# Optimization experiments

Measured on AMD Instinct MI355X. Metric: run time of the kernel, lower is better.

The kernel has to match this reference:

```python
import jax, jax.numpy as jnp
import numpy as np

N_NODES = 100000
N_EDGES = 3200000
ALPHA_KCL = 1.0
ALPHA_KVL = 1.0
EPS = 1e-6


def setup_inputs() -> dict:
    key = jax.random.key(0)
    k1, k2, k3, k4 = jax.random.split(key, 4)
    node_features = jax.random.normal(k1, (N_NODES, 4), dtype=jnp.float32)
    edge_index = jax.random.randint(k2, (2, N_EDGES), 0, N_NODES, dtype=jnp.int64)
    edge_logits = jax.random.normal(k3, (N_EDGES,), dtype=jnp.float32)
    edge_params = jax.random.uniform(k4, (N_EDGES, 2), dtype=jnp.float32)
    return {
        "node_features": node_features,
        "edge_index": edge_index,
        "edge_logits": edge_logits,
        "edge_params": edge_params,
    }


def reference(node_features, edge_index, edge_logits, edge_params):
    n_nodes = node_features.shape[0]
    edge_probs = jax.nn.sigmoid(edge_logits)  # [E]
    src = edge_index[0]  # [E]
    dst = edge_index[1]  # [E]
    v = node_features[:, 0]  # [N] voltage column
    # per-edge current: |v_src - v_dst| / (R + X + eps) * prob
    v_diff = jnp.abs(v[src] - v[dst])
    impedance = edge_params[:, 0] + edge_params[:, 1]
    current = v_diff / (impedance + EPS) * edge_probs  # [E]
    # KCL: each edge subtracts its current at src, adds at dst
    node_sum = (
        jax.ops.segment_sum(current, dst, num_segments=n_nodes)
        - jax.ops.segment_sum(current, src, num_segments=n_nodes)
    )  # [N]
    kcl_loss = jnp.mean(node_sum ** 2)
    # KVL (simplified): mean of per-column unbiased variance of edge_params
    kvl_loss = jnp.var(edge_params, axis=0, ddof=1).mean()
    return ALPHA_KCL * kcl_loss + ALPHA_KVL * kvl_loss
```

## Files before the change

### kernel.cpp

```cpp
#include <hip/hip_runtime.h>
#include <math.h>

#define N_NODES 100000
#define N_EDGES 3200000
#define EPS_F 1e-6f

#define GS_N     80000
#define GNB      256
#define GB_PAIRS (N_EDGES / 2 / GNB)

#define SLICE_N 33336
#define NSLICE  3
#define NCHUNK  64
#define C_PAIRS (N_EDGES / 2 / NCHUNK)
#define SBATCH  16

#define NVARB   6250
#define NKCLB   391

#define PK_OFF    64
#define PART_OFF  (PK_OFF + 2 * N_EDGES)
#define W_OFF     PART_OFF
#define V_OFF     (PART_OFF + N_EDGES / 2)
#define VARP_OFF  (PART_OFF + NCHUNK * N_NODES)
#define KCLP_OFF  (VARP_OFF + 4 * NVARB)
#define WS_FLOATS (KCLP_OFF + NKCLB + 64)

__device__ __forceinline__ float wave_reduce(float v) {
    #pragma unroll
    for (int off = 32; off > 0; off >>= 1) v += __shfl_down(v, off, 64);
    return v;
}

__device__ __forceinline__ void fadd_agent(float* p, float v) {
    unsafeAtomicAdd(p, v);
}

__device__ __forceinline__ unsigned short f2bf(float f) {
    unsigned u = __float_as_uint(f);
    unsigned r = ((u >> 16) & 1u) + 0x7FFFu;
    return (unsigned short)((u + r) >> 16);
}
__device__ __forceinline__ float bf2f(unsigned short h) {
    return __uint_as_float(((unsigned)h) << 16);
}

__global__ __launch_bounds__(256) void prep_kernel(
    const float*  __restrict__ nf,
    const void*   __restrict__ eidx,
    const float*  __restrict__ logits,
    const float2* __restrict__ params,
    float*        __restrict__ ws)
{
    __shared__ float red[4][4];
    const int* i32 = (const int*)eidx;

    int any = 0;
    #pragma unroll
    for (int k = 1; k < 32; k += 2) any |= i32[k];
    const bool is32 = (any != 0);

    const int t = blockIdx.x * blockDim.x + threadIdx.x;

    int2 sp, dp;
    if (is32) {
        sp = ((const int2*)i32)[t];
        dp = ((const int2*)(i32 + N_EDGES))[t];
    } else {
        const int4 a = ((const int4*)i32)[t];
        const int4 b = ((const int4*)(i32 + 2 * N_EDGES))[t];
        sp = make_int2(a.x, a.z);
        dp = make_int2(b.x, b.z);
    }
    int4 pk;
    pk.x = (int)((unsigned)sp.x | ((unsigned)dp.x << 17));
    pk.y = (int)(((unsigned)dp.x) >> 15);
    pk.z = (int)((unsigned)sp.y | ((unsigned)dp.y << 17));
    pk.w = (int)(((unsigned)dp.y) >> 15);
    ((int4*)(ws + PK_OFF))[t] = pk;

    const float4 pp = ((const float4*)params)[t];
    const float2 lg = ((const float2*)logits)[t];
    const float w0 = (1.0f / (1.0f + __expf(-lg.x))) / (pp.x + pp.y + EPS_F);
    const float w1 = (1.0f / (1.0f + __expf(-lg.y))) / (pp.z + pp.w + EPS_F);
    ((unsigned*)(ws + W_OFF))[t] = (unsigned)f2bf(w0) | ((unsigned)f2bf(w1) << 16);

    if (t < N_NODES) ws[V_OFF + t] = nf[t * 4];

    float s0 = pp.x + pp.z;
    float s1 = pp.y + pp.w;
    float q0 = pp.x * pp.x + pp.z * pp.z;
    float q1 = pp.y * pp.y + pp.w * pp.w;

    s0 = wave_reduce(s0); s1 = wave_reduce(s1);
    q0 = wave_reduce(q0); q1 = wave_reduce(q1);

    const int wid = threadIdx.x >> 6;
    if ((threadIdx.x & 63) == 0) {
        red[wid][0] = s0; red[wid][1] = s1; red[wid][2] = q0; red[wid][3] = q1;
    }
    __syncthreads();
    if (threadIdx.x == 0) {
        float4 o;
        o.x = red[0][0] + red[1][0] + red[2][0] + red[3][0];
        o.y = red[0][1] + red[1][1] + red[2][1] + red[3][1];
        o.z = red[0][2] + red[1][2] + red[2][2] + red[3][2];
        o.w = red[0][3] + red[1][3] + red[2][3] + red[3][3];
        ((float4*)(ws + VARP_OFF))[blockIdx.x] = o;
    }
}

__global__ __launch_bounds__(1024) void gather_kernel(float* __restrict__ ws)
{
    __shared__ unsigned vlds32[GS_N / 2];

    const float*  vtab = ws + V_OFF;
    const float2* v2   = (const float2*)vtab;
    for (int j = threadIdx.x; j < GS_N / 2; j += 1024) {
        const float2 f = v2[j];
        vlds32[j] = (unsigned)f2bf(f.x) | ((unsigned)f2bf(f.y) << 16);
    }
    __syncthreads();
    const unsigned short* vl = (const unsigned short*)vlds32;

    int4*           pk = (int4*)(ws + PK_OFF);
    const unsigned* ww = (const unsigned*)(ws + W_OFF);

    const int p0   = blockIdx.x * GB_PAIRS;
    const int p1   = p0 + GB_PAIRS;
    const int base = p0 + (int)threadIdx.x;

    int4     q[8];
    unsigned wv[8];
    #pragma unroll
    for (int k = 0; k < 8; ++k) {
        int p = base + k * 1024;
        p = (p < p1) ? p : (p1 - 1);
        q[k]  = pk[p];
        wv[k] = ww[p];
    }
    #pragma unroll
    for (int k = 0; k < 8; ++k) {
        const int p = base + k * 1024;
        if (p < p1) {
            const unsigned lo0 = (unsigned)q[k].x, hi0 = (unsigned)q[k].y;
            const unsigned lo1 = (unsigned)q[k].z, hi1 = (unsigned)q[k].w;
            const int s0 = (int)(lo0 & 0x1FFFFu);
            const int d0 = (int)((lo0 >> 17) | ((hi0 & 3u) << 15));
            const int s1 = (int)(lo1 & 0x1FFFFu);
            const int d1 = (int)((lo1 >> 17) | ((hi1 & 3u) << 15));
            const float vs0 = (s0 < GS_N) ? bf2f(vl[s0]) : vtab[s0];
            const float vd0 = (d0 < GS_N) ? bf2f(vl[d0]) : vtab[d0];
            const float vs1 = (s1 < GS_N) ? bf2f(vl[s1]) : vtab[s1];
            const float vd1 = (d1 < GS_N) ? bf2f(vl[d1]) : vtab[d1];
            const float c0 = fabsf(vs0 - vd0) * bf2f((unsigned short)(wv[k] & 0xFFFF));
            const float c1 = fabsf(vs1 - vd1) * bf2f((unsigned short)(wv[k] >> 16));
            q[k].y = (int)((hi0 & 3u) | ((unsigned)f2bf(c0) << 2));
            q[k].w = (int)((hi1 & 3u) | ((unsigned)f2bf(c1) << 2));
            pk[p] = q[k];
        }
    }
}

__global__ __launch_bounds__(1024) void scatter_kernel(float* __restrict__ ws)
{
    __shared__ float bins[SLICE_N];

    const int c  = blockIdx.x & (NCHUNK - 1);
    const int s  = blockIdx.x >> 6;
    const unsigned lo = (unsigned)(s * SLICE_N);

    for (int j = threadIdx.x; j < SLICE_N / 4; j += 1024)
        ((float4*)bins)[j] = make_float4(0.f, 0.f, 0.f, 0.f);
    __syncthreads();

    const int4* pk = (const int4*)(ws + PK_OFF);

    const int p0 = c * C_PAIRS;
    const int p1 = p0 + C_PAIRS;

    for (int base = p0 + (int)threadIdx.x; base < p1; base += 1024 * SBATCH) {
        int4 q[SBATCH];
        #pragma unroll
        for (int k = 0; k < SBATCH; ++k) {
            int p = base + k * 1024;
            p = (p < p1) ? p : (p1 - 1);
            q[k] = pk[p];
        }
        #pragma unroll
        for (int k = 0; k < SBATCH; ++k) {
            const int p = base + k * 1024;
            if (p < p1) {
                const unsigned lo0 = (unsigned)q[k].x, hi0 = (unsigned)q[k].y;
                const unsigned lo1 = (unsigned)q[k].z, hi1 = (unsigned)q[k].w;
                const unsigned s0 = (lo0 & 0x1FFFFu) - lo;
                const unsigned d0 = ((lo0 >> 17) | ((hi0 & 3u) << 15)) - lo;
                const unsigned s1 = (lo1 & 0x1FFFFu) - lo;
                const unsigned d1 = ((lo1 >> 17) | ((hi1 & 3u) << 15)) - lo;
                const float c0 = bf2f((unsigned short)((hi0 >> 2) & 0xFFFFu));
                const float c1 = bf2f((unsigned short)((hi1 >> 2) & 0xFFFFu));
                if (d0 < SLICE_N) atomicAdd(&bins[d0],  c0);
                if (s0 < SLICE_N) atomicAdd(&bins[s0], -c0);
                if (d1 < SLICE_N) atomicAdd(&bins[d1],  c1);
                if (s1 < SLICE_N) atomicAdd(&bins[s1], -c1);
            }
        }
    }
    __syncthreads();

    const int n4 = ((int)(N_NODES - lo) < SLICE_N ? (int)(N_NODES - lo) : SLICE_N) / 4;
    float4* pt4 = (float4*)(ws + PART_OFF + (size_t)c * N_NODES + lo);
    for (int j = threadIdx.x; j < n4; j += 1024)
        pt4[j] = ((const float4*)bins)[j];
}

__global__ __launch_bounds__(256) void kcl_kernel(float* __restrict__ ws)
{
    __shared__ float red[4];
    const int i = blockIdx.x * blockDim.x + threadIdx.x;
    float acc = 0.f;
    if (i < N_NODES) {
        const float* p = ws + PART_OFF + i;
        float s = 0.f;
        #pragma unroll 8
        for (int c = 0; c < NCHUNK; ++c) s += p[(size_t)c * N_NODES];
        acc = s * s;
    }
    acc = wave_reduce(acc);
    if ((threadIdx.x & 63) == 0) red[threadIdx.x >> 6] = acc;
    __syncthreads();
    if (threadIdx.x == 0)
        ws[KCLP_OFF + blockIdx.x] = red[0] + red[1] + red[2] + red[3];
}

__global__ __launch_bounds__(1024) void final_kernel(
    const float* __restrict__ ws, float* __restrict__ out)
{
    __shared__ float red[16][5];
    float s0 = 0.f, s1 = 0.f, q0 = 0.f, q1 = 0.f, k = 0.f;

    const float4* vp = (const float4*)(ws + VARP_OFF);
    for (int i = threadIdx.x; i < NVARB; i += 1024) {
        const float4 v = vp[i];
        s0 += v.x; s1 += v.y; q0 += v.z; q1 += v.w;
    }
    for (int i = threadIdx.x; i < NKCLB; i += 1024) k += ws[KCLP_OFF + i];

    s0 = wave_reduce(s0); s1 = wave_reduce(s1);
    q0 = wave_reduce(q0); q1 = wave_reduce(q1);
    k  = wave_reduce(k);

    const int wid = threadIdx.x >> 6;
    if ((threadIdx.x & 63) == 0) {
        red[wid][0] = s0; red[wid][1] = s1; red[wid][2] = q0;
        red[wid][3] = q1; red[wid][4] = k;
    }
    __syncthreads();
    if (threadIdx.x == 0) {
        float a0 = 0.f, a1 = 0.f, a2 = 0.f, a3 = 0.f, a4 = 0.f;
        #pragma unroll
        for (int w = 0; w < 16; ++w) {
            a0 += red[w][0]; a1 += red[w][1]; a2 += red[w][2];
            a3 += red[w][3]; a4 += red[w][4];
        }
        const float n    = (float)N_EDGES;
        const float var0 = (a2 - a0 * a0 / n) / (n - 1.0f);
        const float var1 = (a3 - a1 * a1 / n) / (n - 1.0f);
        out[0] = a4 / (float)N_NODES + 0.5f * (var0 + var1);
    }
}

#define FB_NODE_OFF 64
__global__ __launch_bounds__(256) void edge_kernel_fb(
    const float*  __restrict__ nf,
    const void*   __restrict__ eidx,
    const float*  __restrict__ logits,
    const float2* __restrict__ params,
    float*        __restrict__ ws)
{
    const int*       i32 = (const int*)eidx;
    const long long* i64 = (const long long*)eidx;
    int any = 0;
    #pragma unroll
    for (int k = 1; k < 32; k += 2) any |= i32[k];
    const bool is32 = (any != 0);

    float* node_sum = ws + FB_NODE_OFF;
    float* acc      = ws + 1;

    float s0 = 0.f, s1 = 0.f, q0 = 0.f, q1 = 0.f;
    const int tid    = blockIdx.x * blockDim.x + threadIdx.x;
    const int stride = gridDim.x * blockDim.x;
    for (int i = tid; i < N_EDGES; i += stride) {
        int src, dst;
        if (is32) { src = i32[i]; dst = i32[N_EDGES + i]; }
        else      { src = (int)i64[i]; dst = (int)i64[N_EDGES + i]; }
        const float2 ep = params[i];
        const float  p  = 1.0f / (1.0f + __expf(-logits[i]));
        const float cur = fabsf(nf[src * 4] - nf[dst * 4]) / (ep.x + ep.y + EPS_F) * p;
        fadd_agent(node_sum + dst,  cur);
        fadd_agent(node_sum + src, -cur);
        s0 += ep.x; s1 += ep.y; q0 += ep.x * ep.x; q1 += ep.y * ep.y;
    }
    s0 = wave_reduce(s0); s1 = wave_reduce(s1);
    q0 = wave_reduce(q0); q1 = wave_reduce(q1);
    if ((threadIdx.x & 63) == 0) {
        fadd_agent(acc + 0, s0); fadd_agent(acc + 1, s1);
        fadd_agent(acc + 2, q0); fadd_agent(acc + 3, q1);
    }
}

__global__ __launch_bounds__(256) void kcl_kernel_fb(float* __restrict__ ws)
{
    const float* node_sum = ws + FB_NODE_OFF;
    float acc = 0.f;
    const int tid    = blockIdx.x * blockDim.x + threadIdx.x;
    const int stride = gridDim.x * blockDim.x;
    for (int i = tid; i < N_NODES; i += stride) {
        const float v = node_sum[i];
        acc += v * v;
    }
    acc = wave_reduce(acc);
    if ((threadIdx.x & 63) == 0) fadd_agent(ws + 5, acc);
}

__global__ void final_kernel_fb(const float* __restrict__ ws, float* __restrict__ out)
{
    const float s0 = ws[1], s1 = ws[2], q0 = ws[3], q1 = ws[4], k = ws[5];
    const float n  = (float)N_EDGES;
    const float var0 = (q0 - s0 * s0 / n) / (n - 1.0f);
    const float var1 = (q1 - s1 * s1 / n) / (n - 1.0f);
    out[0] = k / (float)N_NODES + 0.5f * (var0 + var1);
}

extern "C" void kernel_launch(void* const* d_in, const int* in_sizes, int n_in,
                              void* d_out, int out_size, void* d_ws, size_t ws_size,
                              hipStream_t stream) {
    const float*  nf     = (const float*)d_in[0];
    const void*   eidx   = d_in[1];
    const float*  logits = (const float*)d_in[2];
    const float2* params = (const float2*)d_in[3];
    float* ws  = (float*)d_ws;
    float* out = (float*)d_out;

    const size_t need = (size_t)WS_FLOATS * sizeof(float);

    if (ws_size >= need) {
        prep_kernel<<<NVARB, 256, 0, stream>>>(nf, eidx, logits, params, ws);
        gather_kernel<<<GNB, 1024, 0, stream>>>(ws);
        scatter_kernel<<<NCHUNK * NSLICE, 1024, 0, stream>>>(ws);
        kcl_kernel<<<NKCLB, 256, 0, stream>>>(ws);
        final_kernel<<<1, 1024, 0, stream>>>(ws, out);
    } else {
        hipMemsetAsync(d_ws, 0, 256 + (size_t)N_NODES * sizeof(float), stream);
        edge_kernel_fb<<<2048, 256, 0, stream>>>(nf, eidx, logits, params, ws);
        kcl_kernel_fb<<<200, 256, 0, stream>>>(ws);
        final_kernel_fb<<<1, 1, 0, stream>>>(ws, out);
    }
}
```

Baseline: 183.9 us.

## Fuse voltage gather into prep kernel and retune scatter slices

Removes the separate gather kernel: the prep kernel now reads node voltages straight from node_features by random gather and packs the bf16 current alongside the indices in one pass. This drops a full round trip over the packed edge array and the weight and voltage staging buffers, plus one launch. The scatter stage is retuned to five slices of 20000 nodes with a smaller batch, trading more passes over the edge list for a smaller LDS footprint per block. The uncached random gathers from the strided node_features array may cost more than the old LDS-cached bf16 table, and the extra slice passes add edge-array reads.

New measurement: 194.8 us. 6.0% more time.

```diff
diff --git a/kernel.cpp b/kernel.cpp
--- a/kernel.cpp
+++ b/kernel.cpp
@@ -5,23 +5,17 @@
 #define N_EDGES 3200000
 #define EPS_F 1e-6f
 
-#define GS_N     80000
-#define GNB      256
-#define GB_PAIRS (N_EDGES / 2 / GNB)
-
-#define SLICE_N 33336
-#define NSLICE  3
+#define SLICE_N 20000
+#define NSLICE  5
 #define NCHUNK  64
 #define C_PAIRS (N_EDGES / 2 / NCHUNK)
-#define SBATCH  16
+#define SBATCH  8
 
 #define NVARB   6250
 #define NKCLB   391
 
 #define PK_OFF    64
 #define PART_OFF  (PK_OFF + 2 * N_EDGES)
-#define W_OFF     PART_OFF
-#define V_OFF     (PART_OFF + N_EDGES / 2)
 #define VARP_OFF  (PART_OFF + NCHUNK * N_NODES)
 #define KCLP_OFF  (VARP_OFF + 4 * NVARB)
 #define WS_FLOATS (KCLP_OFF + NKCLB + 64)
@@ -72,20 +66,25 @@
         sp = make_int2(a.x, a.z);
         dp = make_int2(b.x, b.z);
     }
-    int4 pk;
-    pk.x = (int)((unsigned)sp.x | ((unsigned)dp.x << 17));
-    pk.y = (int)(((unsigned)dp.x) >> 15);
-    pk.z = (int)((unsigned)sp.y | ((unsigned)dp.y << 17));
-    pk.w = (int)(((unsigned)dp.y) >> 15);
-    ((int4*)(ws + PK_OFF))[t] = pk;
+
+    const float vs0 = nf[sp.x * 4];
+    const float vd0 = nf[dp.x * 4];
+    const float vs1 = nf[sp.y * 4];
+    const float vd1 = nf[dp.y * 4];
 
     const float4 pp = ((const float4*)params)[t];
     const float2 lg = ((const float2*)logits)[t];
     const float w0 = (1.0f / (1.0f + __expf(-lg.x))) / (pp.x + pp.y + EPS_F);
     const float w1 = (1.0f / (1.0f + __expf(-lg.y))) / (pp.z + pp.w + EPS_F);
-    ((unsigned*)(ws + W_OFF))[t] = (unsigned)f2bf(w0) | ((unsigned)f2bf(w1) << 16);
-
-    if (t < N_NODES) ws[V_OFF + t] = nf[t * 4];
+    const float c0 = fabsf(vs0 - vd0) * w0;
+    const float c1 = fabsf(vs1 - vd1) * w1;
+
+    int4 pk;
+    pk.x = (int)((unsigned)sp.x | ((unsigned)dp.x << 17));
+    pk.y = (int)((((unsigned)dp.x) >> 15) | ((unsigned)f2bf(c0) << 2));
+    pk.z = (int)((unsigned)sp.y | ((unsigned)dp.y << 17));
+    pk.w = (int)((((unsigned)dp.y) >> 15) | ((unsigned)f2bf(c1) << 2));
+    ((int4*)(ws + PK_OFF))[t] = pk;
 
     float s0 = pp.x + pp.z;
     float s1 = pp.y + pp.w;
@@ -107,58 +106,6 @@
         o.z = red[0][2] + red[1][2] + red[2][2] + red[3][2];
         o.w = red[0][3] + red[1][3] + red[2][3] + red[3][3];
         ((float4*)(ws + VARP_OFF))[blockIdx.x] = o;
-    }
-}
-
-__global__ __launch_bounds__(1024) void gather_kernel(float* __restrict__ ws)
-{
-    __shared__ unsigned vlds32[GS_N / 2];
-
-    const float*  vtab = ws + V_OFF;
-    const float2* v2   = (const float2*)vtab;
-    for (int j = threadIdx.x; j < GS_N / 2; j += 1024) {
-        const float2 f = v2[j];
-        vlds32[j] = (unsigned)f2bf(f.x) | ((unsigned)f2bf(f.y) << 16);
-    }
-    __syncthreads();
-    const unsigned short* vl = (const unsigned short*)vlds32;
-
-    int4*           pk = (int4*)(ws + PK_OFF);
-    const unsigned* ww = (const unsigned*)(ws + W_OFF);
-
-    const int p0   = blockIdx.x * GB_PAIRS;
-    const int p1   = p0 + GB_PAIRS;
-    const int base = p0 + (int)threadIdx.x;
-
-    int4     q[8];
-    unsigned wv[8];
-    #pragma unroll
-    for (int k = 0; k < 8; ++k) {
-        int p = base + k * 1024;
-        p = (p < p1) ? p : (p1 - 1);
-        q[k]  = pk[p];
-        wv[k] = ww[p];
-    }
-    #pragma unroll
-    for (int k = 0; k < 8; ++k) {
-        const int p = base + k * 1024;
-        if (p < p1) {
-            const unsigned lo0 = (unsigned)q[k].x, hi0 = (unsigned)q[k].y;
-            const unsigned lo1 = (unsigned)q[k].z, hi1 = (unsigned)q[k].w;
-            const int s0 = (int)(lo0 & 0x1FFFFu);
-            const int d0 = (int)((lo0 >> 17) | ((hi0 & 3u) << 15));
-            const int s1 = (int)(lo1 & 0x1FFFFu);
-            const int d1 = (int)((lo1 >> 17) | ((hi1 & 3u) << 15));
-            const float vs0 = (s0 < GS_N) ? bf2f(vl[s0]) : vtab[s0];
-            const float vd0 = (d0 < GS_N) ? bf2f(vl[d0]) : vtab[d0];
-            const float vs1 = (s1 < GS_N) ? bf2f(vl[s1]) : vtab[s1];
-            const float vd1 = (d1 < GS_N) ? bf2f(vl[d1]) : vtab[d1];
-            const float c0 = fabsf(vs0 - vd0) * bf2f((unsigned short)(wv[k] & 0xFFFF));
-            const float c1 = fabsf(vs1 - vd1) * bf2f((unsigned short)(wv[k] >> 16));
-            q[k].y = (int)((hi0 & 3u) | ((unsigned)f2bf(c0) << 2));
-            q[k].w = (int)((hi1 & 3u) | ((unsigned)f2bf(c1) << 2));
-            pk[p] = q[k];
-        }
     }
 }
 
@@ -208,9 +155,8 @@
     }
     __syncthreads();
 
-    const int n4 = ((int)(N_NODES - lo) < SLICE_N ? (int)(N_NODES - lo) : SLICE_N) / 4;
     float4* pt4 = (float4*)(ws + PART_OFF + (size_t)c * N_NODES + lo);
-    for (int j = threadIdx.x; j < n4; j += 1024)
+    for (int j = threadIdx.x; j < SLICE_N / 4; j += 1024)
         pt4[j] = ((const float4*)bins)[j];
 }
 
@@ -347,7 +293,6 @@
 
     if (ws_size >= need) {
         prep_kernel<<<NVARB, 256, 0, stream>>>(nf, eidx, logits, params, ws);
-        gather_kernel<<<GNB, 1024, 0, stream>>>(ws);
         scatter_kernel<<<NCHUNK * NSLICE, 1024, 0, stream>>>(ws);
         kcl_kernel<<<NKCLB, 256, 0, stream>>>(ws);
         final_kernel<<<1, 1024, 0, stream>>>(ws, out);
```
